# Kernel tuning notes

Measured on AMD Instinct MI355X. Metric: run time of the kernel, lower is better.

## Reference

```python
import jax, jax.numpy as jnp
import numpy as np
from jax.scipy.special import logsumexp

B, L, DIN, H, NL, E = 32, 1024, 2048, 1024, 21, 768
LN_EPS = 1e-5

def setup_inputs() -> dict:
    key = jax.random.key(0)
    ks = jax.random.split(key, 8)
    return {
        "seq_feats": jax.random.normal(ks[0], (B, L, DIN), jnp.float32),
        "labels": jax.random.randint(ks[1], (B, L), 0, NL),
        "attention_mask": jnp.ones((B, L), jnp.bool_),
        "W_tok": jax.random.normal(ks[2], (DIN, H), jnp.float32) * 0.02,
        "ln_gamma": jnp.ones((H,), jnp.float32),
        "ln_beta": jnp.zeros((H,), jnp.float32),
        "label_table": jax.random.normal(ks[3], (NL, E), jnp.float32) * 0.02,
        "W_lab": jax.random.normal(ks[4], (E, H), jnp.float32) * 0.02,
        "temperature": jnp.float32(10.0),
        "start_trans": jax.random.uniform(ks[5], (NL,), jnp.float32, -0.1, 0.1),
        "end_trans": jax.random.uniform(ks[6], (NL,), jnp.float32, -0.1, 0.1),
        "trans": jax.random.uniform(ks[7], (NL, NL), jnp.float32, -0.1, 0.1),
    }

def _crf_nll(logits, labels, mask, start_trans, end_trans, trans):
    # torchcrf CRF(batch_first=True), reduction='mean': loss = -mean_b llh_b
    mf = mask.astype(logits.dtype)  # (B,L)
    # --- numerator: score of the gold path ---
    emit = jnp.take_along_axis(logits, labels[..., None], axis=-1)[..., 0]  # (B,L)
    score = start_trans[labels[:, 0]] + emit[:, 0]
    score = score + (emit[:, 1:] * mf[:, 1:]).sum(-1)
    score = score + (trans[labels[:, :-1], labels[:, 1:]] * mf[:, 1:]).sum(-1)
    last_idx = mask.sum(-1).astype(jnp.int32) - 1  # (B,)
    last_tag = jnp.take_along_axis(labels, last_idx[:, None], axis=1)[:, 0]
    score = score + end_trans[last_tag]
    # --- denominator: log partition via forward algorithm (lax.scan over time) ---
    alpha0 = start_trans[None, :] + logits[:, 0]  # (B,NL)
    def step(alpha, xs):
        emit_t, m_t = xs  # (B,NL), (B,)
        new = logsumexp(alpha[:, :, None] + trans[None, :, :] + emit_t[:, None, :], axis=1)
        return jnp.where(m_t[:, None], new, alpha), None
    xs = (jnp.moveaxis(logits[:, 1:], 1, 0), jnp.moveaxis(mask[:, 1:], 1, 0))
    alpha, _ = jax.lax.scan(step, alpha0, xs)
    logZ = logsumexp(alpha + end_trans[None, :], axis=-1)  # (B,)
    return -(score - logZ).mean()

def reference(seq_feats, labels, attention_mask, W_tok, ln_gamma, ln_beta,
              label_table, W_lab, temperature, start_trans, end_trans, trans):
    # token_proj: Linear(no bias) -> LayerNorm -> GELU (exact) -> Dropout(eval=no-op)
    h = seq_feats @ W_tok  # (B,L,H)
    mu = h.mean(-1, keepdims=True)
    var = h.var(-1, keepdims=True)
    h = (h - mu) / jnp.sqrt(var + LN_EPS) * ln_gamma + ln_beta
    token_h = jax.nn.gelu(h, approximate=False)
    label_h = label_table @ W_lab  # (NL,H)
    logits = jnp.einsum('blh,nh->bln', token_h, label_h) * temperature
    loss = _crf_nll(logits, labels, attention_mask, start_trans, end_trans, trans)
    return logits, loss
```

## Files before the change

kernel.cpp:

```cpp
#include <hip/hip_runtime.h>
#include <math.h>

typedef __attribute__((ext_vector_type(8))) short bf16x8;
typedef __attribute__((ext_vector_type(4))) float f32x4;
typedef unsigned short u16;

#define Bsz 32
#define Lsz 1024
#define DIN 2048
#define Hsz 1024
#define NLB 21
#define CCH 64
#define TCH 16

__device__ __forceinline__ float b2f(u16 u) {
  union { unsigned int i; float f; } v; v.i = ((unsigned int)u) << 16; return v.f;
}
__device__ __forceinline__ u16 f2b(float f) {
  union { float f; unsigned int i; } v; v.f = f;
  unsigned int r = v.i + 0x7fffu + ((v.i >> 16) & 1u);
  return (u16)(r >> 16);
}

__global__ void k_convA(const float* __restrict__ in, u16* __restrict__ out, int n4) {
  int idx = blockIdx.x * blockDim.x + threadIdx.x;
  int stride = gridDim.x * blockDim.x;
  const float4* in4 = (const float4*)in;
  ushort4* out4 = (ushort4*)out;
  for (int i = idx; i < n4; i += stride) {
    float4 v = in4[i];
    ushort4 o;
    o.x = f2b(v.x); o.y = f2b(v.y); o.z = f2b(v.z); o.w = f2b(v.w);
    out4[i] = o;
  }
}

__global__ void k_convWT(const float* __restrict__ W, u16* __restrict__ Wt) {
  __shared__ float tile[64][65];
  const int ntile = blockIdx.x & 15;
  const int ktile = blockIdx.x >> 4;
  const int n0 = ntile * 64, k0 = ktile * 64;
  const int tid = threadIdx.x;
#pragma unroll
  for (int i = 0; i < 16; ++i) {
    int lin = i * 256 + tid;
    int r = lin >> 6, c = lin & 63;
    tile[r][c] = W[(size_t)(k0 + r) * Hsz + n0 + c];
  }
  __syncthreads();
#pragma unroll
  for (int i = 0; i < 16; ++i) {
    int lin = i * 256 + tid;
    int r = lin >> 6, c = lin & 63;
    Wt[(size_t)(n0 + r) * DIN + k0 + c] = f2b(tile[c][r]);
  }
}

__global__ void k_trW(const float* __restrict__ WL, float* __restrict__ WLt) {
  __shared__ float tile[64][65];
  const int nt = blockIdx.x & 15;
  const int et = blockIdx.x >> 4;
  const int n0 = nt * 64, e0 = et * 64;
  const int tid = threadIdx.x;
#pragma unroll
  for (int i = 0; i < 16; ++i) {
    int lin = i * 256 + tid;
    int r = lin >> 6, c = lin & 63;
    tile[r][c] = WL[(size_t)(e0 + r) * Hsz + n0 + c];
  }
  __syncthreads();
#pragma unroll
  for (int i = 0; i < 16; ++i) {
    int lin = i * 256 + tid;
    int r = lin >> 6, c = lin & 63;
    WLt[(size_t)(n0 + r) * 768 + e0 + c] = tile[c][r];
  }
}

__global__ __launch_bounds__(256) void k_labelh(const float* __restrict__ LT, const float* __restrict__ WLt,
                                                u16* __restrict__ LH) {
  const int tid = threadIdx.x;
  const int lane = tid & 63;
  const int wave = tid >> 6;
  const int wid = blockIdx.x * 4 + wave;
  const int row = wid >> 10;
  const int col = wid & 1023;
  const float4* a4 = (const float4*)(LT + (size_t)row * 768);
  const float4* b4 = (const float4*)(WLt + (size_t)col * 768);
  float p = 0.f;
#pragma unroll
  for (int it = 0; it < 3; ++it) {
    float4 a = a4[it * 64 + lane];
    float4 b = b4[it * 64 + lane];
    p += a.x * b.x + a.y * b.y + a.z * b.z + a.w * b.w;
  }
#pragma unroll
  for (int o = 32; o; o >>= 1) p += __shfl_xor(p, o);
  if (lane == 0) LH[(size_t)row * Hsz + col] = f2b(p);
}

__global__ __launch_bounds__(256) void k_gemm(const u16* __restrict__ A, const u16* __restrict__ Bt,
                                              u16* __restrict__ H) {
  __shared__ u16 sA[128 * 64];
  __shared__ u16 sB[128 * 64];
  const int tid = threadIdx.x;
  const int lane = tid & 63;
  const int wave = tid >> 6;
  const int m0 = (blockIdx.x >> 3) * 128;
  const int n0 = (blockIdx.x & 7) * 128;
  const int wm = (wave >> 1) * 64;
  const int wn = (wave & 1) * 64;

  f32x4 acc[4][4];
#pragma unroll
  for (int i = 0; i < 4; ++i)
#pragma unroll
    for (int j = 0; j < 4; ++j) acc[i][j] = (f32x4){0.f, 0.f, 0.f, 0.f};

  for (int k0 = 0; k0 < DIN; k0 += 64) {
#pragma unroll
    for (int q = 0; q < 4; ++q) {
      int idx = q * 256 + tid;
      int row = idx >> 3;
      int cl = (idx & 7) ^ (row & 7);
      const u16* ga = A + (size_t)(m0 + row) * DIN + k0 + cl * 8;
      __builtin_amdgcn_global_load_lds((const __attribute__((address_space(1))) void*)ga,
                                       (__attribute__((address_space(3))) void*)&sA[idx * 8], 16, 0, 0);
      const u16* gb = Bt + (size_t)(n0 + row) * DIN + k0 + cl * 8;
      __builtin_amdgcn_global_load_lds((const __attribute__((address_space(1))) void*)gb,
                                       (__attribute__((address_space(3))) void*)&sB[idx * 8], 16, 0, 0);
    }
    __syncthreads();
#pragma unroll
    for (int ks = 0; ks < 2; ++ks) {
      bf16x8 af[4], bfr[4];
      const int quad = lane >> 4;
      const int ck = ks * 4 + quad;
#pragma unroll
      for (int t = 0; t < 4; ++t) {
        int m = wm + t * 16 + (lane & 15);
        af[t] = *(const bf16x8*)&sA[m * 64 + ((ck ^ (m & 7)) * 8)];
        int n = wn + t * 16 + (lane & 15);
        bfr[t] = *(const bf16x8*)&sB[n * 64 + ((ck ^ (n & 7)) * 8)];
      }
#pragma unroll
      for (int i = 0; i < 4; ++i)
#pragma unroll
        for (int j = 0; j < 4; ++j)
          acc[i][j] = __builtin_amdgcn_mfma_f32_16x16x32_bf16(af[i], bfr[j], acc[i][j], 0, 0, 0);
    }
    __syncthreads();
  }
#pragma unroll
  for (int i = 0; i < 4; ++i) {
#pragma unroll
    for (int j = 0; j < 4; ++j) {
      int col = n0 + wn + j * 16 + (lane & 15);
      int r0 = m0 + wm + i * 16 + ((lane >> 4) << 2);
#pragma unroll
      for (int r = 0; r < 4; ++r) H[(size_t)(r0 + r) * Hsz + col] = f2b(acc[i][j][r]);
    }
  }
}

__global__ __launch_bounds__(256) void k_head(const u16* __restrict__ Hb, const u16* __restrict__ LH,
                                              const float* __restrict__ gamma, const float* __restrict__ beta,
                                              const float* __restrict__ tempp, float* __restrict__ logits) {
  __shared__ u16 sLH[NLB * Hsz];
  __shared__ float sTok[Hsz];
  __shared__ float sRed[8];
  const int tid = threadIdx.x;
  const int lane = tid & 63;
  const int wave = tid >> 6;
  {
    const uint4* src = (const uint4*)LH;
    uint4* dst = (uint4*)sLH;
    for (int i = tid; i < (NLB * Hsz) / 8; i += 256) dst[i] = src[i];
  }
  const float4 gv = ((const float4*)gamma)[tid];
  const float4 bv = ((const float4*)beta)[tid];
  const float T = tempp[0];
  __syncthreads();
  const int tok0 = blockIdx.x * 8;
  for (int tk = 0; tk < 8; ++tk) {
    const int tok = tok0 + tk;
    ushort4 hv = ((const ushort4*)(Hb + (size_t)tok * Hsz))[tid];
    float x0 = b2f(hv.x), x1 = b2f(hv.y), x2 = b2f(hv.z), x3 = b2f(hv.w);
    float s = x0 + x1 + x2 + x3;
    float s2 = x0 * x0 + x1 * x1 + x2 * x2 + x3 * x3;
#pragma unroll
    for (int o = 32; o; o >>= 1) { s += __shfl_xor(s, o); s2 += __shfl_xor(s2, o); }
    if (lane == 0) { sRed[wave] = s; sRed[4 + wave] = s2; }
    __syncthreads();
    s = sRed[0] + sRed[1] + sRed[2] + sRed[3];
    s2 = sRed[4] + sRed[5] + sRed[6] + sRed[7];
    const float mu = s * (1.0f / 1024.0f);
    const float var = s2 * (1.0f / 1024.0f) - mu * mu;
    const float rstd = rsqrtf(var + 1e-5f);
    float y[4] = {(x0 - mu) * rstd * gv.x + bv.x, (x1 - mu) * rstd * gv.y + bv.y,
                  (x2 - mu) * rstd * gv.z + bv.z, (x3 - mu) * rstd * gv.w + bv.w};
#pragma unroll
    for (int i = 0; i < 4; ++i) {
      float yy = y[i];
      sTok[tid * 4 + i] = 0.5f * yy * (1.0f + erff(yy * 0.70710678118654752f));
    }
    __syncthreads();
    for (int n = wave; n < NLB; n += 4) {
      const float2* th2 = (const float2*)sTok;
      const u16* lrow = sLH + n * Hsz;
      float p = 0.f;
#pragma unroll
      for (int it = 0; it < 8; ++it) {
        int ip = it * 64 + lane;
        float2 t2 = th2[ip];
        unsigned int lu = *(const unsigned int*)(lrow + ip * 2);
        p += t2.x * b2f((u16)(lu & 0xffffu)) + t2.y * b2f((u16)(lu >> 16));
      }
#pragma unroll
      for (int o = 32; o; o >>= 1) p += __shfl_xor(p, o);
      if (lane == 0) logits[(size_t)tok * NLB + n] = p * T;
    }
    __syncthreads();
  }
}

__global__ __launch_bounds__(256) void k_crf1(const float* __restrict__ logits,
                                              const float* __restrict__ trans,
                                              float* __restrict__ Mexp, float* __restrict__ Rlog,
                                              float* __restrict__ loss) {
  __shared__ float sEt[NLB * 24];
  const int tid = threadIdx.x;
  for (int idx = tid; idx < NLB * NLB; idx += 256) {
    int jj = idx / NLB, kk = idx % NLB;
    sEt[jj * 24 + kk] = __expf(trans[kk * NLB + jj]);
  }
  if (blockIdx.x == 0 && tid == 0) *loss = 0.f;
  __syncthreads();

  const int lane = tid & 63;
  const int wave = tid >> 6;
  const int pg = lane >= 42 ? 2 : (lane >= 21 ? 1 : 0);
  const int i0 = lane - pg * 21;
  const bool maskv0 = (lane < 63);
  const int i = i0 > 20 ? 20 : i0;
  const int prob_raw = (blockIdx.x * 4 + wave) * 3 + pg;
  const bool maskv = maskv0 && (prob_raw < Bsz * CCH);
  const int prob = prob_raw < Bsz * CCH ? prob_raw : Bsz * CCH - 1;
  const int b = prob >> 6;
  const int c = prob & 63;
  const int t0 = 1 + c * TCH;
  const float* lg = logits + (size_t)b * Lsz * NLB;

  float P[NLB], rlog = 0.f;
#pragma unroll
  for (int j = 0; j < NLB; ++j)
    P[j] = sEt[j * 24 + i] * __expf(lg[t0 * NLB + j]);
  {
    float m = P[0];
#pragma unroll
    for (int j = 1; j < NLB; ++j) m = fmaxf(m, P[j]);
    rlog = __logf(m);
    float r = 1.0f / m;
#pragma unroll
    for (int j = 0; j < NLB; ++j) P[j] *= r;
  }

  for (int tt = 1; tt < TCH; ++tt) {
    const int t = t0 + tt;
    if (t >= Lsz) break;
    float q[NLB];
#pragma unroll
    for (int j = 0; j < NLB; ++j) {
      const float* e = &sEt[j * 24];
      float4 e0 = *(const float4*)(e);
      float4 e1 = *(const float4*)(e + 4);
      float4 e2 = *(const float4*)(e + 8);
      float4 e3 = *(const float4*)(e + 12);
      float4 e4 = *(const float4*)(e + 16);
      float e5 = e[20];
      float s = P[0] * e0.x + P[1] * e0.y + P[2] * e0.z + P[3] * e0.w
              + P[4] * e1.x + P[5] * e1.y + P[6] * e1.z + P[7] * e1.w
              + P[8] * e2.x + P[9] * e2.y + P[10] * e2.z + P[11] * e2.w
              + P[12] * e3.x + P[13] * e3.y + P[14] * e3.z + P[15] * e3.w
              + P[16] * e4.x + P[17] * e4.y + P[18] * e4.z + P[19] * e4.w
              + P[20] * e5;
      q[j] = s * __expf(lg[t * NLB + j]);
    }
    float m = q[0];
#pragma unroll
    for (int j = 1; j < NLB; ++j) m = fmaxf(m, q[j]);
    rlog += __logf(m);
    float r = 1.0f / m;
#pragma unroll
    for (int j = 0; j < NLB; ++j) P[j] = q[j] * r;
  }

  if (maskv) {
    float* mo = Mexp + ((size_t)prob * NLB + i) * NLB;
#pragma unroll
    for (int j = 0; j < NLB; ++j) mo[j] = P[j];
    Rlog[(size_t)prob * NLB + i] = rlog;
  }
}

__global__ __launch_bounds__(64) void k_crf2(const float* __restrict__ logits, const int* __restrict__ labels,
                                             const float* __restrict__ startt, const float* __restrict__ endt,
                                             const float* __restrict__ trans,
                                             const float* __restrict__ Mexp, const float* __restrict__ Rlog,
                                             float* __restrict__ loss) {
  const int b = blockIdx.x;
  const int lane = threadIdx.x;
  const float* lg = logits + (size_t)b * Lsz * NLB;
  const int* lab = labels + (size_t)b * Lsz;

  float sc = 0.f;
  for (int t = lane; t < Lsz; t += 64) {
    int lt = lab[t];
    sc += lg[t * NLB + lt];
    if (t > 0) sc += trans[lab[t - 1] * NLB + lt];
  }
#pragma unroll
  for (int o = 32; o; o >>= 1) sc += __shfl_xor(sc, o);
  if (lane == 0) sc += startt[lab[0]] + endt[lab[Lsz - 1]];
  const float score = __shfl(sc, 0);

  const bool act = (lane < NLB);
  const int jc = act ? lane : NLB - 1;
  float a0 = act ? (startt[lane] + lg[lane]) : -INFINITY;
  float m = a0;
#pragma unroll
  for (int o = 32; o; o >>= 1) m = fmaxf(m, __shfl_xor(m, o));
  float p = act ? __expf(a0 - m) : 0.f;
  float macc = m;

  for (int c = 0; c < CCH; ++c) {
    const size_t prob = (size_t)b * CCH + c;
    float li = __logf(p) + Rlog[prob * NLB + jc];
    if (!act) li = -INFINITY;
    float S = li;
#pragma unroll
    for (int o = 32; o; o >>= 1) S = fmaxf(S, __shfl_xor(S, o));
    float w = __expf(li - S);
    const float* mc = Mexp + prob * (NLB * NLB) + jc;
    float q0 = 0.f, q1 = 0.f, q2 = 0.f;
#pragma unroll
    for (int ii = 0; ii < NLB; ii += 3) {
      q0 += __shfl(w, ii) * mc[ii * NLB];
      if (ii + 1 < NLB) q1 += __shfl(w, ii + 1) * mc[(ii + 1) * NLB];
      if (ii + 2 < NLB) q2 += __shfl(w, ii + 2) * mc[(ii + 2) * NLB];
    }
    float q = act ? (q0 + q1 + q2) : 0.f;
    float mx = q;
#pragma unroll
    for (int o = 32; o; o >>= 1) mx = fmaxf(mx, __shfl_xor(mx, o));
    p = q * (1.0f / mx);
    macc += S + __logf(mx);
  }

  float z = act ? p * __expf(endt[lane]) : 0.f;
#pragma unroll
  for (int o = 32; o; o >>= 1) z += __shfl_xor(z, o);
  if (lane == 0) {
    float logZ = macc + __logf(z);
    atomicAdd(loss, (logZ - score) * (1.0f / 32.0f));
  }
}

extern "C" void kernel_launch(void* const* d_in, const int* in_sizes, int n_in,
                              void* d_out, int out_size, void* d_ws, size_t ws_size,
                              hipStream_t stream) {
  const float* seq   = (const float*)d_in[0];
  const int*   labs  = (const int*)d_in[1];
  const float* Wtok  = (const float*)d_in[3];
  const float* gamma = (const float*)d_in[4];
  const float* beta  = (const float*)d_in[5];
  const float* LT    = (const float*)d_in[6];
  const float* WL    = (const float*)d_in[7];
  const float* temp  = (const float*)d_in[8];
  const float* st    = (const float*)d_in[9];
  const float* en    = (const float*)d_in[10];
  const float* tr    = (const float*)d_in[11];

  float* logits = (float*)d_out;
  float* loss   = logits + (size_t)Bsz * Lsz * NLB;

  char* ws = (char*)d_ws;
  u16* Abf   = (u16*)(ws);
  u16* Hbf   = (u16*)(ws + 134217728);
  float* WLt = (float*)(ws + 134217728);
  u16* Wt    = (u16*)(ws + 201326592);
  u16* LH    = (u16*)(ws + 205520896);
  float* Mexp = (float*)(ws);
  float* Rlog = (float*)(ws + 3612672);

  k_convA <<<dim3(4096), dim3(256), 0, stream>>>(seq, Abf, (Bsz * Lsz * DIN) / 4);
  k_convWT<<<dim3(512),  dim3(256), 0, stream>>>(Wtok, Wt);
  k_trW   <<<dim3(192),  dim3(256), 0, stream>>>(WL, WLt);
  k_labelh<<<dim3(5376), dim3(256), 0, stream>>>(LT, WLt, LH);
  k_gemm  <<<dim3(2048), dim3(256), 0, stream>>>(Abf, Wt, Hbf);
  k_head  <<<dim3(4096), dim3(256), 0, stream>>>(Hbf, LH, gamma, beta, temp, logits);
  k_crf1  <<<dim3(171),  dim3(256), 0, stream>>>(logits, tr, Mexp, Rlog, loss);
  k_crf2  <<<dim3(32),   dim3(64),  0, stream>>>(logits, labs, st, en, tr, Mexp, Rlog, loss);
}
```

Baseline: 842.1 us.

## Rewrite head kernel to use MFMA with per-wave token tiles and swizzled LDS

The LayerNorm+GELU+label projection head is restructured so each wave handles 16 tokens. Row statistics are computed in registers with lane shuffles instead of block-wide reductions and barriers, and the 21-label dot products are done with bf16 MFMA 16x16x32 instructions against a zero-padded, XOR-swizzled LDS copy of the label matrix. This removes the per-token syncthreads and the scalar dot-product loop and cuts the grid from 4096 to 512 blocks. In exchange, GELU outputs are rounded to bf16 before the matmul, and each token row is read twice from global memory.

After: 728.0 us. -13.5%, faster.

```diff
diff --git a/kernel.cpp b/kernel.cpp
--- a/kernel.cpp
+++ b/kernel.cpp
@@ -166,61 +166,70 @@
 __global__ __launch_bounds__(256) void k_head(const u16* __restrict__ Hb, const u16* __restrict__ LH,
                                               const float* __restrict__ gamma, const float* __restrict__ beta,
                                               const float* __restrict__ tempp, float* __restrict__ logits) {
-  __shared__ u16 sLH[NLB * Hsz];
-  __shared__ float sTok[Hsz];
-  __shared__ float sRed[8];
+  __shared__ u16 sLH[32 * Hsz];
   const int tid = threadIdx.x;
   const int lane = tid & 63;
   const int wave = tid >> 6;
-  {
-    const uint4* src = (const uint4*)LH;
-    uint4* dst = (uint4*)sLH;
-    for (int i = tid; i < (NLB * Hsz) / 8; i += 256) dst[i] = src[i];
-  }
-  const float4 gv = ((const float4*)gamma)[tid];
-  const float4 bv = ((const float4*)beta)[tid];
+  for (int id = tid; id < 32 * 64; id += 256) {
+    int n = id >> 6, c = id & 63;
+    uint4 v = (uint4){0u, 0u, 0u, 0u};
+    if (n < NLB) v = *(const uint4*)(LH + (size_t)n * Hsz + c * 8);
+    *(uint4*)&sLH[((n << 6) | ((c & 56) | ((c ^ n) & 7))) * 8] = v;
+  }
   const float T = tempp[0];
   __syncthreads();
-  const int tok0 = blockIdx.x * 8;
-  for (int tk = 0; tk < 8; ++tk) {
-    const int tok = tok0 + tk;
-    ushort4 hv = ((const ushort4*)(Hb + (size_t)tok * Hsz))[tid];
-    float x0 = b2f(hv.x), x1 = b2f(hv.y), x2 = b2f(hv.z), x3 = b2f(hv.w);
-    float s = x0 + x1 + x2 + x3;
-    float s2 = x0 * x0 + x1 * x1 + x2 * x2 + x3 * x3;
-#pragma unroll
-    for (int o = 32; o; o >>= 1) { s += __shfl_xor(s, o); s2 += __shfl_xor(s2, o); }
-    if (lane == 0) { sRed[wave] = s; sRed[4 + wave] = s2; }
-    __syncthreads();
-    s = sRed[0] + sRed[1] + sRed[2] + sRed[3];
-    s2 = sRed[4] + sRed[5] + sRed[6] + sRed[7];
-    const float mu = s * (1.0f / 1024.0f);
-    const float var = s2 * (1.0f / 1024.0f) - mu * mu;
-    const float rstd = rsqrtf(var + 1e-5f);
-    float y[4] = {(x0 - mu) * rstd * gv.x + bv.x, (x1 - mu) * rstd * gv.y + bv.y,
-                  (x2 - mu) * rstd * gv.z + bv.z, (x3 - mu) * rstd * gv.w + bv.w};
-#pragma unroll
-    for (int i = 0; i < 4; ++i) {
-      float yy = y[i];
-      sTok[tid * 4 + i] = 0.5f * yy * (1.0f + erff(yy * 0.70710678118654752f));
-    }
-    __syncthreads();
-    for (int n = wave; n < NLB; n += 4) {
-      const float2* th2 = (const float2*)sTok;
-      const u16* lrow = sLH + n * Hsz;
-      float p = 0.f;
-#pragma unroll
-      for (int it = 0; it < 8; ++it) {
-        int ip = it * 64 + lane;
-        float2 t2 = th2[ip];
-        unsigned int lu = *(const unsigned int*)(lrow + ip * 2);
-        p += t2.x * b2f((u16)(lu & 0xffffu)) + t2.y * b2f((u16)(lu >> 16));
-      }
-#pragma unroll
-      for (int o = 32; o; o >>= 1) p += __shfl_xor(p, o);
-      if (lane == 0) logits[(size_t)tok * NLB + n] = p * T;
-    }
-    __syncthreads();
+
+  const int m = lane & 15;
+  const int q = lane >> 4;
+  const int tok = blockIdx.x * 64 + wave * 16 + m;
+  const u16* arow = Hb + (size_t)tok * Hsz;
+
+  float s = 0.f, s2 = 0.f;
+  for (int kc = 0; kc < 32; ++kc) {
+    bf16x8 v = *(const bf16x8*)(arow + kc * 32 + q * 8);
+#pragma unroll
+    for (int j = 0; j < 8; ++j) {
+      float x = b2f(((const u16*)&v)[j]);
+      s += x; s2 += x * x;
+    }
+  }
+  s += __shfl_xor(s, 16);  s += __shfl_xor(s, 32);
+  s2 += __shfl_xor(s2, 16); s2 += __shfl_xor(s2, 32);
+  const float mu = s * (1.0f / 1024.0f);
+  const float rstd = rsqrtf(s2 * (1.0f / 1024.0f) - mu * mu + 1e-5f);
+
+  f32x4 acc0 = (f32x4){0.f, 0.f, 0.f, 0.f};
+  f32x4 acc1 = (f32x4){0.f, 0.f, 0.f, 0.f};
+  const int nr = lane & 15;
+  for (int kc = 0; kc < 32; ++kc) {
+    const int k = kc * 32 + q * 8;
+    bf16x8 v = *(const bf16x8*)(arow + k);
+    float4 g0 = *(const float4*)(gamma + k);
+    float4 g1 = *(const float4*)(gamma + k + 4);
+    float4 e0 = *(const float4*)(beta + k);
+    float4 e1 = *(const float4*)(beta + k + 4);
+    float gs[8] = {g0.x, g0.y, g0.z, g0.w, g1.x, g1.y, g1.z, g1.w};
+    float bs[8] = {e0.x, e0.y, e0.z, e0.w, e1.x, e1.y, e1.z, e1.w};
+    bf16x8 a;
+#pragma unroll
+    for (int j = 0; j < 8; ++j) {
+      float x = b2f(((const u16*)&v)[j]);
+      float y = (x - mu) * rstd * gs[j] + bs[j];
+      float gl = 0.5f * y * (1.0f + erff(y * 0.70710678118654752f));
+      ((u16*)&a)[j] = f2b(gl);
+    }
+    const int c = kc * 4 + q;
+    const int cs = (c & 56) | ((c ^ nr) & 7);
+    bf16x8 b0 = *(const bf16x8*)&sLH[((nr << 6) | cs) * 8];
+    bf16x8 b1 = *(const bf16x8*)&sLH[(((16 + nr) << 6) | cs) * 8];
+    acc0 = __builtin_amdgcn_mfma_f32_16x16x32_bf16(a, b0, acc0, 0, 0, 0);
+    acc1 = __builtin_amdgcn_mfma_f32_16x16x32_bf16(a, b1, acc1, 0, 0, 0);
+  }
+  const int rbase = blockIdx.x * 64 + wave * 16 + q * 4;
+#pragma unroll
+  for (int r = 0; r < 4; ++r) {
+    logits[(size_t)(rbase + r) * NLB + nr] = acc0[r] * T;
+    if (nr < 5) logits[(size_t)(rbase + r) * NLB + 16 + nr] = acc1[r] * T;
   }
 }
 
@@ -398,7 +407,7 @@
   k_trW   <<<dim3(192),  dim3(256), 0, stream>>>(WL, WLt);
   k_labelh<<<dim3(5376), dim3(256), 0, stream>>>(LT, WLt, LH);
   k_gemm  <<<dim3(2048), dim3(256), 0, stream>>>(Abf, Wt, Hbf);
-  k_head  <<<dim3(4096), dim3(256), 0, stream>>>(Hbf, LH, gamma, beta, temp, logits);
+  k_head  <<<dim3(512),  dim3(256), 0, stream>>>(Hbf, LH, gamma, beta, temp, logits);
   k_crf1  <<<dim3(171),  dim3(256), 0, stream>>>(logits, tr, Mexp, Rlog, loss);
   k_crf2  <<<dim3(32),   dim3(64),  0, stream>>>(logits, labs, st, en, tr, Mexp, Rlog, loss);
 }
```
